# Optimization experiments

Measured on AMD Instinct MI355X. Metric: run time of the kernel, lower is better.

The kernel has to match this reference:

```python
import jax, jax.numpy as jnp
import numpy as np

N_NODES = 100000
N_EDGES = 3200000
IN_FEATS = 7
HIDDEN = 32


def setup_inputs() -> dict:
    key = jax.random.key(0)
    ks = jax.random.split(key, 9)
    inp = {
        "x_t": jax.random.normal(ks[0], (N_NODES, IN_FEATS), dtype=jnp.float32),
        "x_t_dt": jax.random.normal(ks[1], (N_NODES, IN_FEATS), dtype=jnp.float32),
        "edge_index": jax.random.randint(ks[2], (2, N_EDGES), 0, N_NODES, dtype=jnp.int64),
        # node_encoder: Linear(in_feats, hidden)
        "W_enc": jax.random.normal(ks[3], (IN_FEATS, HIDDEN), dtype=jnp.float32) * 0.1,
        "b_enc": jnp.zeros((HIDDEN,), dtype=jnp.float32),
        # GCNConv(hidden, hidden): weight + bias
        "W_gcn": jax.random.normal(ks[4], (HIDDEN, HIDDEN), dtype=jnp.float32) * 0.1,
        "b_gcn": jnp.zeros((HIDDEN,), dtype=jnp.float32),
        # edge_classifier: Linear(2*hidden, 1)
        "W_edge": jax.random.normal(ks[5], (2 * HIDDEN, 1), dtype=jnp.float32) * 0.1,
        "b_edge": jnp.zeros((1,), dtype=jnp.float32),
    }
    return inp


def reference(x_t, x_t_dt, edge_index, W_enc, b_enc, W_gcn, b_gcn, W_edge, b_edge):
    N = x_t.shape[0]
    src, dst = edge_index[0], edge_index[1]

    # node encoder + relu
    h = jax.nn.relu(x_t @ W_enc + b_enc)

    # GCNConv (PyG default): add self-loops, symmetric normalization
    h = h @ W_gcn  # [N, H]
    deg = jax.ops.segment_sum(jnp.ones(src.shape[0], h.dtype), dst, num_segments=N) + 1.0
    dinv = jax.lax.rsqrt(deg)  # deg^-1/2, [N]
    norm = dinv[src] * dinv[dst]  # [E]
    agg = jax.ops.segment_sum(h[src] * norm[:, None], dst, num_segments=N)
    # self-loop contribution: dinv[i]*dinv[i]*h[i]
    h = agg + h * (dinv * dinv)[:, None] + b_gcn
    h = jax.nn.relu(h)
    # dropout: identity in eval mode

    # edge scorer: gather src/dst, concat, linear, sigmoid
    edge_repr = jnp.concatenate([h[src], h[dst]], axis=-1)  # [E, 2H]
    scores = jax.nn.sigmoid(edge_repr @ W_edge + b_edge).reshape(-1)  # [E]
    return scores
```

## Files before the change

### kernel.cpp

```cpp
#include <hip/hip_runtime.h>
#include <hip/hip_fp16.h>
#include <math.h>

#define NN 100000
#define NE 3200000
#define IN_F 7
#define H 32

#define BSH 9
#define BSPAN 512
#define NBUK ((NN + BSPAN - 1) / BSPAN)
#define EPB 8192

__global__ __launch_bounds__(256) void k_encode(const float* __restrict__ x,
                                                const float* __restrict__ Wenc,
                                                const float* __restrict__ benc,
                                                const float* __restrict__ Wgcn,
                                                uint4* __restrict__ hW_h4) {
    __shared__ float sWe[IN_F * H];
    __shared__ float sb[H];
    __shared__ float sWg[H * H];
    for (int i = threadIdx.x; i < IN_F * H; i += 256) sWe[i] = Wenc[i];
    for (int i = threadIdx.x; i < H; i += 256) sb[i] = benc[i];
    for (int i = threadIdx.x; i < H * H; i += 256) sWg[i] = Wgcn[i];
    __syncthreads();

    int n = blockIdx.x * 256 + threadIdx.x;
    if (n >= NN) return;

    float xl[IN_F];
#pragma unroll
    for (int j = 0; j < IN_F; ++j) xl[j] = x[n * IN_F + j];

    float h[H];
#pragma unroll
    for (int k = 0; k < H; ++k) {
        float a = sb[k];
#pragma unroll
        for (int j = 0; j < IN_F; ++j) a = fmaf(xl[j], sWe[j * H + k], a);
        h[k] = fmaxf(a, 0.f);
    }
    float a[H];
#pragma unroll
    for (int k = 0; k < H; ++k) {
        float s = 0.f;
#pragma unroll
        for (int j = 0; j < H; ++j) s = fmaf(h[j], sWg[j * H + k], s);
        a[k] = s;
    }
    uint4 pk[4];
    __half2* hp = reinterpret_cast<__half2*>(pk);
#pragma unroll
    for (int k = 0; k < 16; ++k) hp[k] = __floats2half2_rn(a[2 * k], a[2 * k + 1]);
#pragma unroll
    for (int q = 0; q < 4; ++q) hW_h4[n * 4 + q] = pk[q];
}

__global__ __launch_bounds__(1024) void k_bhist(const int* __restrict__ dst,
                                                int* __restrict__ bucket_cnt) {
    __shared__ int cnt[NBUK];
    for (int i = threadIdx.x; i < NBUK; i += 1024) cnt[i] = 0;
    __syncthreads();
    int base = blockIdx.x * EPB;
#pragma unroll
    for (int r = 0; r < EPB / 1024; ++r) {
        int e = base + r * 1024 + threadIdx.x;
        if (e < NE) atomicAdd(&cnt[dst[e] >> BSH], 1);
    }
    __syncthreads();
    for (int i = threadIdx.x; i < NBUK; i += 1024)
        if (cnt[i]) atomicAdd(&bucket_cnt[i], cnt[i]);
}

__global__ __launch_bounds__(256) void k_bscan(const int* __restrict__ bucket_cnt,
                                               int* __restrict__ bucket_base,
                                               int* __restrict__ bucket_cur) {
    __shared__ int tmp[256];
    int t = threadIdx.x;
    int v = (t < NBUK) ? bucket_cnt[t] : 0;
    tmp[t] = v;
    __syncthreads();
    for (int off = 1; off < 256; off <<= 1) {
        int u = (t >= off) ? tmp[t - off] : 0;
        __syncthreads();
        tmp[t] += u;
        __syncthreads();
    }
    int ex = tmp[t] - v;
    if (t < NBUK) {
        bucket_base[t] = ex;
        bucket_cur[t] = ex;
    }
    if (t == NBUK - 1) bucket_base[NBUK] = ex + v;
}

__global__ __launch_bounds__(1024) void k_bscatter(const int* __restrict__ src,
                                                   const int* __restrict__ dst,
                                                   int* __restrict__ bucket_cur,
                                                   unsigned int* __restrict__ pairs) {
    __shared__ int cnt[NBUK];
    __shared__ int cbase[NBUK];
    for (int i = threadIdx.x; i < NBUK; i += 1024) cnt[i] = 0;
    __syncthreads();
    int base = blockIdx.x * EPB;
#pragma unroll
    for (int r = 0; r < EPB / 1024; ++r) {
        int e = base + r * 1024 + threadIdx.x;
        if (e < NE) atomicAdd(&cnt[dst[e] >> BSH], 1);
    }
    __syncthreads();
    for (int i = threadIdx.x; i < NBUK; i += 1024) {
        int c = cnt[i];
        cbase[i] = c ? atomicAdd(&bucket_cur[i], c) : 0;
    }
    __syncthreads();
    for (int i = threadIdx.x; i < NBUK; i += 1024) cnt[i] = 0;
    __syncthreads();
#pragma unroll
    for (int r = 0; r < EPB / 1024; ++r) {
        int e = base + r * 1024 + threadIdx.x;
        if (e < NE) {
            int d = dst[e];
            int b = d >> BSH;
            int lp = atomicAdd(&cnt[b], 1);
            pairs[cbase[b] + lp] = ((unsigned int)src[e] << BSH) | (unsigned int)(d & (BSPAN - 1));
        }
    }
}

__global__ __launch_bounds__(1024) void k_bfill(const unsigned int* __restrict__ pairs,
                                                const int* __restrict__ bucket_base,
                                                int* __restrict__ row_ptr,
                                                float* __restrict__ dinv,
                                                int* __restrict__ csr_src) {
    __shared__ int cnt[BSPAN];
    __shared__ int pre[BSPAN];
    int b = blockIdx.x;
    int ebeg = bucket_base[b], eend = bucket_base[b + 1];
    int t = threadIdx.x;
    for (int i = t; i < BSPAN; i += 1024) cnt[i] = 0;
    __syncthreads();
    for (int e = ebeg + t; e < eend; e += 1024)
        atomicAdd(&cnt[pairs[e] & (BSPAN - 1)], 1);
    __syncthreads();
    if (t < BSPAN) pre[t] = cnt[t];
    __syncthreads();
    for (int off = 1; off < BSPAN; off <<= 1) {
        int v = (t < BSPAN && t >= off) ? pre[t - off] : 0;
        __syncthreads();
        if (t < BSPAN) pre[t] += v;
        __syncthreads();
    }
    int nbase = b * BSPAN;
    if (t < BSPAN) {
        int node = nbase + t;
        if (node < NN) {
            row_ptr[node] = ebeg + pre[t] - cnt[t];
            dinv[node] = rsqrtf((float)cnt[t] + 1.0f);
        }
    }
    if (b == NBUK - 1 && t == 0) row_ptr[NN] = NE;
    __syncthreads();
    if (t < BSPAN) cnt[t] = ebeg + pre[t] - cnt[t];
    __syncthreads();
    for (int e = ebeg + t; e < eend; e += 1024) {
        unsigned int p = pairs[e];
        int pos = atomicAdd(&cnt[p & (BSPAN - 1)], 1);
        csr_src[pos] = (int)(p >> BSH);
    }
}

__global__ __launch_bounds__(256) void k_gather(const int* __restrict__ row_ptr,
                                                const int* __restrict__ csr_src,
                                                const float* __restrict__ dinv,
                                                const uint4* __restrict__ hW_h4,
                                                const float* __restrict__ bgcn,
                                                uint4* __restrict__ h2_h4) {
    int tid = blockIdx.x * 256 + threadIdx.x;
    int n = tid >> 2;
    int c = tid & 3;
    if (n >= NN) return;
    float dn = dinv[n];
    int beg = row_ptr[n], end = row_ptr[n + 1];
    float acc[8];
#pragma unroll
    for (int i = 0; i < 8; ++i) acc[i] = 0.f;
    for (int k = beg; k < end; ++k) {
        int s = csr_src[k];
        float nrm = dinv[s] * dn;
        uint4 v = hW_h4[s * 4 + c];
        const __half2* hp = reinterpret_cast<const __half2*>(&v);
#pragma unroll
        for (int i = 0; i < 4; ++i) {
            float2 f = __half22float2(hp[i]);
            acc[2 * i]     = fmaf(f.x, nrm, acc[2 * i]);
            acc[2 * i + 1] = fmaf(f.y, nrm, acc[2 * i + 1]);
        }
    }
    float sl = dn * dn;
    uint4 w = hW_h4[n * 4 + c];
    const __half2* wp = reinterpret_cast<const __half2*>(&w);
    uint4 pk;
    __half2* op = reinterpret_cast<__half2*>(&pk);
#pragma unroll
    for (int i = 0; i < 4; ++i) {
        float2 f = __half22float2(wp[i]);
        float r0 = fmaxf(acc[2 * i]     + f.x * sl + bgcn[c * 8 + 2 * i],     0.f);
        float r1 = fmaxf(acc[2 * i + 1] + f.y * sl + bgcn[c * 8 + 2 * i + 1], 0.f);
        op[i] = __floats2half2_rn(r0, r1);
    }
    h2_h4[n * 4 + c] = pk;
}

__global__ __launch_bounds__(256) void k_score(const int* __restrict__ src,
                                               const int* __restrict__ dst,
                                               const uint4* __restrict__ h2_h4,
                                               const float* __restrict__ We,
                                               const float* __restrict__ be,
                                               float* __restrict__ out) {
    __shared__ float sW[2 * H];
    __shared__ float sB;
    if (threadIdx.x < 2 * H) sW[threadIdx.x] = We[threadIdx.x];
    if (threadIdx.x == 0) sB = be[0];
    __syncthreads();

    int tid = blockIdx.x * 256 + threadIdx.x;
    int e = tid >> 2;
    int c = tid & 3;
    if (e >= NE) return;
    int s = src[e];
    int d = dst[e];
    uint4 av = h2_h4[s * 4 + c];
    uint4 bv = h2_h4[d * 4 + c];
    const __half2* ap = reinterpret_cast<const __half2*>(&av);
    const __half2* bp = reinterpret_cast<const __half2*>(&bv);
    float acc = 0.f;
#pragma unroll
    for (int i = 0; i < 4; ++i) {
        float2 fa = __half22float2(ap[i]);
        float2 fb = __half22float2(bp[i]);
        acc = fmaf(fa.x, sW[c * 8 + 2 * i],         acc);
        acc = fmaf(fa.y, sW[c * 8 + 2 * i + 1],     acc);
        acc = fmaf(fb.x, sW[H + c * 8 + 2 * i],     acc);
        acc = fmaf(fb.y, sW[H + c * 8 + 2 * i + 1], acc);
    }
    acc += __shfl_xor(acc, 1, 4);
    acc += __shfl_xor(acc, 2, 4);
    if (c == 0) {
        float sc = 1.0f / (1.0f + __expf(-(acc + sB)));
        __builtin_nontemporal_store(sc, &out[e]);
    }
}

extern "C" void kernel_launch(void* const* d_in, const int* in_sizes, int n_in,
                              void* d_out, int out_size, void* d_ws, size_t ws_size,
                              hipStream_t stream) {
    const float* x_t   = (const float*)d_in[0];
    const int*   eidx  = (const int*)d_in[2];
    const float* Wenc  = (const float*)d_in[3];
    const float* benc  = (const float*)d_in[4];
    const float* Wgcn  = (const float*)d_in[5];
    const float* bgcn  = (const float*)d_in[6];
    const float* Wedge = (const float*)d_in[7];
    const float* bedge = (const float*)d_in[8];
    float* out = (float*)d_out;

    const int* src = eidx;
    const int* dst = eidx + NE;

    char* ws = (char*)d_ws;
    if (ws_size < 33000000) return;

    uint4*        hW_h4    = (uint4*)(ws);
    unsigned int* pairs    = (unsigned int*)(ws + 6400064);
    uint4*        h2_h4    = (uint4*)(ws + 6400064);
    int*          csr_src  = (int*)(ws + 19200128);
    int*          row_ptr  = (int*)(ws + 32000192);
    float*        dinv     = (float*)(ws + 32400256);
    int*          bucket_cnt  = (int*)(ws + 32800320);
    int*          bucket_base = (int*)(ws + 32801280);
    int*          bucket_cur  = (int*)(ws + 32802304);

    hipMemsetAsync(bucket_cnt, 0, NBUK * sizeof(int), stream);

    int ebks = (NE + EPB - 1) / EPB;
    k_encode<<<(NN + 255) / 256, 256, 0, stream>>>(x_t, Wenc, benc, Wgcn, hW_h4);
    k_bhist<<<ebks, 1024, 0, stream>>>(dst, bucket_cnt);
    k_bscan<<<1, 256, 0, stream>>>(bucket_cnt, bucket_base, bucket_cur);
    k_bscatter<<<ebks, 1024, 0, stream>>>(src, dst, bucket_cur, pairs);
    k_bfill<<<NBUK, 1024, 0, stream>>>(pairs, bucket_base, row_ptr, dinv, csr_src);
    k_gather<<<(NN * 4 + 255) / 256, 256, 0, stream>>>(row_ptr, csr_src, dinv, hW_h4, bgcn, h2_h4);
    k_score<<<((size_t)NE * 4 + 255) / 256, 256, 0, stream>>>(src, dst, h2_h4, Wedge, bedge, out);
}
```

Baseline: 298.5 us.

## Precompute per-node edge-classifier dot products and fuse them into the gather kernel

The edge linear layer splits into a source half and a destination half, so each node's two dot products with W_edge are computed once in the aggregation kernel and stored as a float2. The edge kernel then reads two scalars per edge instead of two 64-byte fp16 hidden vectors, and uses one thread per edge instead of four. This cuts per-edge gather traffic and arithmetic, and it drops the fp16 rounding of h2 before the dot product. The workspace layout is shifted to make room for the per-node array.

Result: faster. 265.6 us (-11.0%).

```diff
diff --git a/kernel.cpp b/kernel.cpp
--- a/kernel.cpp
+++ b/kernel.cpp
@@ -175,7 +175,8 @@
                                                 const float* __restrict__ dinv,
                                                 const uint4* __restrict__ hW_h4,
                                                 const float* __restrict__ bgcn,
-                                                uint4* __restrict__ h2_h4) {
+                                                const float* __restrict__ We,
+                                                float2* __restrict__ ab) {
     int tid = blockIdx.x * 256 + threadIdx.x;
     int n = tid >> 2;
     int c = tid & 3;
@@ -200,56 +201,34 @@
     float sl = dn * dn;
     uint4 w = hW_h4[n * 4 + c];
     const __half2* wp = reinterpret_cast<const __half2*>(&w);
-    uint4 pk;
-    __half2* op = reinterpret_cast<__half2*>(&pk);
+    float dota = 0.f, dotb = 0.f;
 #pragma unroll
     for (int i = 0; i < 4; ++i) {
         float2 f = __half22float2(wp[i]);
         float r0 = fmaxf(acc[2 * i]     + f.x * sl + bgcn[c * 8 + 2 * i],     0.f);
         float r1 = fmaxf(acc[2 * i + 1] + f.y * sl + bgcn[c * 8 + 2 * i + 1], 0.f);
-        op[i] = __floats2half2_rn(r0, r1);
-    }
-    h2_h4[n * 4 + c] = pk;
-}
-
-__global__ __launch_bounds__(256) void k_score(const int* __restrict__ src,
-                                               const int* __restrict__ dst,
-                                               const uint4* __restrict__ h2_h4,
-                                               const float* __restrict__ We,
-                                               const float* __restrict__ be,
-                                               float* __restrict__ out) {
-    __shared__ float sW[2 * H];
-    __shared__ float sB;
-    if (threadIdx.x < 2 * H) sW[threadIdx.x] = We[threadIdx.x];
-    if (threadIdx.x == 0) sB = be[0];
-    __syncthreads();
-
-    int tid = blockIdx.x * 256 + threadIdx.x;
-    int e = tid >> 2;
-    int c = tid & 3;
+        dota = fmaf(r0, We[c * 8 + 2 * i],         dota);
+        dota = fmaf(r1, We[c * 8 + 2 * i + 1],     dota);
+        dotb = fmaf(r0, We[H + c * 8 + 2 * i],     dotb);
+        dotb = fmaf(r1, We[H + c * 8 + 2 * i + 1], dotb);
+    }
+    dota += __shfl_xor(dota, 1, 4);
+    dota += __shfl_xor(dota, 2, 4);
+    dotb += __shfl_xor(dotb, 1, 4);
+    dotb += __shfl_xor(dotb, 2, 4);
+    if (c == 0) ab[n] = make_float2(dota, dotb);
+}
+
+__global__ __launch_bounds__(256) void k_edge(const int* __restrict__ src,
+                                              const int* __restrict__ dst,
+                                              const float2* __restrict__ ab,
+                                              const float* __restrict__ be,
+                                              float* __restrict__ out) {
+    int e = blockIdx.x * 256 + threadIdx.x;
     if (e >= NE) return;
-    int s = src[e];
-    int d = dst[e];
-    uint4 av = h2_h4[s * 4 + c];
-    uint4 bv = h2_h4[d * 4 + c];
-    const __half2* ap = reinterpret_cast<const __half2*>(&av);
-    const __half2* bp = reinterpret_cast<const __half2*>(&bv);
-    float acc = 0.f;
-#pragma unroll
-    for (int i = 0; i < 4; ++i) {
-        float2 fa = __half22float2(ap[i]);
-        float2 fb = __half22float2(bp[i]);
-        acc = fmaf(fa.x, sW[c * 8 + 2 * i],         acc);
-        acc = fmaf(fa.y, sW[c * 8 + 2 * i + 1],     acc);
-        acc = fmaf(fb.x, sW[H + c * 8 + 2 * i],     acc);
-        acc = fmaf(fb.y, sW[H + c * 8 + 2 * i + 1], acc);
-    }
-    acc += __shfl_xor(acc, 1, 4);
-    acc += __shfl_xor(acc, 2, 4);
-    if (c == 0) {
-        float sc = 1.0f / (1.0f + __expf(-(acc + sB)));
-        __builtin_nontemporal_store(sc, &out[e]);
-    }
+    float logit = ab[src[e]].x + ab[dst[e]].y + be[0];
+    float sc = 1.0f / (1.0f + __expf(-logit));
+    __builtin_nontemporal_store(sc, &out[e]);
 }
 
 extern "C" void kernel_launch(void* const* d_in, const int* in_sizes, int n_in,
@@ -269,17 +248,17 @@
     const int* dst = eidx + NE;
 
     char* ws = (char*)d_ws;
-    if (ws_size < 33000000) return;
+    if (ws_size < 33700000) return;
 
     uint4*        hW_h4    = (uint4*)(ws);
     unsigned int* pairs    = (unsigned int*)(ws + 6400064);
-    uint4*        h2_h4    = (uint4*)(ws + 6400064);
     int*          csr_src  = (int*)(ws + 19200128);
     int*          row_ptr  = (int*)(ws + 32000192);
     float*        dinv     = (float*)(ws + 32400256);
-    int*          bucket_cnt  = (int*)(ws + 32800320);
-    int*          bucket_base = (int*)(ws + 32801280);
-    int*          bucket_cur  = (int*)(ws + 32802304);
+    float2*       ab       = (float2*)(ws + 32800320);
+    int*          bucket_cnt  = (int*)(ws + 33600384);
+    int*          bucket_base = (int*)(ws + 33601344);
+    int*          bucket_cur  = (int*)(ws + 33602368);
 
     hipMemsetAsync(bucket_cnt, 0, NBUK * sizeof(int), stream);
 
@@ -289,6 +268,6 @@
     k_bscan<<<1, 256, 0, stream>>>(bucket_cnt, bucket_base, bucket_cur);
     k_bscatter<<<ebks, 1024, 0, stream>>>(src, dst, bucket_cur, pairs);
     k_bfill<<<NBUK, 1024, 0, stream>>>(pairs, bucket_base, row_ptr, dinv, csr_src);
-    k_gather<<<(NN * 4 + 255) / 256, 256, 0, stream>>>(row_ptr, csr_src, dinv, hW_h4, bgcn, h2_h4);
-    k_score<<<((size_t)NE * 4 + 255) / 256, 256, 0, stream>>>(src, dst, h2_h4, Wedge, bedge, out);
-}
+    k_gather<<<(NN * 4 + 255) / 256, 256, 0, stream>>>(row_ptr, csr_src, dinv, hW_h4, bgcn, Wedge, ab);
+    k_edge<<<(NE + 255) / 256, 256, 0, stream>>>(src, dst, ab, bedge, out);
+}
```
